# Performance work log

Measured on AMD Instinct MI355X. Metric: run time of the kernel, lower is better.

The kernel has to match this reference:

```python
import jax, jax.numpy as jnp
import numpy as np

B = 8
INPUT_DIM = 6670   # upper-triangle of 116x116 FC matrix (AAL atlas)
N = 116
FD = 16
HEADS = (8, 4, 1)
DIMS = (128, 256, 512)
NC = 2
THR = 0.5
EPS = 1e-5


def _glorot(key, shape):
    s = (2.0 / (shape[0] + shape[-1])) ** 0.5
    return jax.random.normal(key, shape, dtype=jnp.float32) * s


def setup_inputs() -> dict:
    key = jax.random.key(0)
    ks = iter(jax.random.split(key, 64))
    inp = {}
    inp['x'] = jax.random.normal(next(ks), (B, INPUT_DIM), dtype=jnp.float32)
    # DynamicGraphBuilder params
    inp['W_gb'] = _glorot(next(ks), (INPUT_DIM, N * N))
    inp['b_gb'] = jnp.zeros((N * N,), jnp.float32)
    inp['fe_W1'] = _glorot(next(ks), (2, 8)); inp['fe_b1'] = jnp.zeros((8,), jnp.float32)
    inp['fe_W2'] = _glorot(next(ks), (8, FD)); inp['fe_b2'] = jnp.zeros((FD,), jnp.float32)
    inp['ln_g'] = jnp.ones((FD,), jnp.float32); inp['ln_b'] = jnp.zeros((FD,), jnp.float32)
    # GATv2 layers
    prev = FD
    for l, (d, h) in enumerate(zip(DIMS, HEADS)):
        inp['Wl%d' % l] = _glorot(next(ks), (prev, h * d))
        inp['bl%d' % l] = jnp.zeros((h * d,), jnp.float32)
        inp['Wr%d' % l] = _glorot(next(ks), (prev, h * d))
        inp['br%d' % l] = jnp.zeros((h * d,), jnp.float32)
        inp['att%d' % l] = _glorot(next(ks), (h, d))
        inp['bias%d' % l] = jnp.zeros((h * d,), jnp.float32)
        prev = h * d
    # classifier
    inp['Wc1'] = _glorot(next(ks), (prev, 256)); inp['bc1'] = jnp.zeros((256,), jnp.float32)
    inp['bn_g'] = jnp.ones((256,), jnp.float32); inp['bn_b'] = jnp.zeros((256,), jnp.float32)
    inp['Wc2'] = _glorot(next(ks), (256, NC)); inp['bc2'] = jnp.zeros((NC,), jnp.float32)
    return inp


def _gatv2(hx, mask_st, Wl, bl, Wr, br, att, bias, heads, out_dim, self_loops):
    # mask_st[b, src, tgt] True if edge src->tgt exists (PyG flow source_to_target)
    Bn, Nn, _ = hx.shape
    if self_loops:  # PyG remove_self_loops + add_self_loops => diag forced present
        mask_st = mask_st | jnp.eye(Nn, dtype=bool)
    xl = (hx @ Wl + bl).reshape(Bn, Nn, heads, out_dim)  # source transform
    xr = (hx @ Wr + br).reshape(Bn, Nn, heads, out_dim)  # target transform
    # pairwise: axis1 = target i, axis2 = source j  -> [B, i, j, h, o]
    z = jax.nn.leaky_relu(xr[:, :, None] + xl[:, None, :], 0.2)
    e = jnp.einsum('bijho,ho->bhij', z, att)  # [B, h, tgt, src]
    m = jnp.swapaxes(mask_st, 1, 2)[:, None]  # [B, 1, tgt, src]
    em = jnp.where(m, e, -1e30)
    emax = jnp.max(em, axis=-1, keepdims=True)
    p = jnp.exp(em - emax) * m  # zero for masked / empty rows
    alpha = p / jnp.maximum(p.sum(-1, keepdims=True), 1e-16)
    out = jnp.einsum('bhij,bjho->biho', alpha, xl).reshape(Bn, Nn, heads * out_dim)
    return out + bias


def _forward(x, W_gb, b_gb, fe_W1, fe_b1, fe_W2, fe_b2, ln_g, ln_b,
             Wl0, bl0, Wr0, br0, att0, bias0,
             Wl1, bl1, Wr1, br1, att1, bias1,
             Wl2, bl2, Wr2, br2, att2, bias2,
             Wc1, bc1, bn_g, bn_b, Wc2, bc2):
    Bn = x.shape[0]
    adj = jax.nn.sigmoid(x @ W_gb + b_gb).reshape(Bn, N, N)
    mask = adj > THR                      # edge (row -> col) exists
    adj_t = jnp.where(mask, adj, 0.0)     # thresholded adjacency
    mu = adj_t.mean(-1)                   # torch mean(dim=1) on [N,N]
    std = jnp.sqrt(jnp.sum((adj_t - mu[..., None]) ** 2, -1) / (N - 1))  # unbiased
    stats = jnp.stack([mu, std], -1)      # [B, N, 2]
    hfe = jax.nn.gelu(stats @ fe_W1 + fe_b1, approximate=False) @ fe_W2 + fe_b2
    lm = hfe.mean(-1, keepdims=True)
    lv = jnp.mean((hfe - lm) ** 2, -1, keepdims=True)
    h = (hfe - lm) / jnp.sqrt(lv + EPS) * ln_g + ln_b  # [B, N, FD]
    convs = [
        (Wl0, bl0, Wr0, br0, att0, bias0, HEADS[0], DIMS[0], False),
        (Wl1, bl1, Wr1, br1, att1, bias1, HEADS[1], DIMS[1], True),
        (Wl2, bl2, Wr2, br2, att2, bias2, HEADS[2], DIMS[2], True),
    ]
    for (Wl, bl, Wr, br, att, bias, hh, dd, sl) in convs:
        h = jax.nn.gelu(_gatv2(h, mask, Wl, bl, Wr, br, att, bias, hh, dd, sl), approximate=False)
    pooled = h.mean(1)                    # global_mean_pool per graph
    c = pooled @ Wc1 + bc1
    c = c / jnp.sqrt(1.0 + EPS) * bn_g + bn_b  # BatchNorm1d eval (running mean 0, var 1)
    c = jax.nn.gelu(c, approximate=False)
    return c @ Wc2 + bc2


def reference(x, W_gb, b_gb, fe_W1, fe_b1, fe_W2, fe_b2, ln_g, ln_b,
              Wl0, bl0, Wr0, br0, att0, bias0,
              Wl1, bl1, Wr1, br1, att1, bias1,
              Wl2, bl2, Wr2, br2, att2, bias2,
              Wc1, bc1, bn_g, bn_b, Wc2, bc2):
    return _forward(x, W_gb, b_gb, fe_W1, fe_b1, fe_W2, fe_b2, ln_g, ln_b,
                    Wl0, bl0, Wr0, br0, att0, bias0,
                    Wl1, bl1, Wr1, br1, att1, bias1,
                    Wl2, bl2, Wr2, br2, att2, bias2,
                    Wc1, bc1, bn_g, bn_b, Wc2, bc2)
```

## Files before the change

kernel.cpp:

```cpp
#include <hip/hip_runtime.h>
#include <math.h>


#define NB 8
#define NN 116
#define NN2 (NN*NN)
#define KIN 6670
#define FD 16
#define KCHUNK 64
#define KSTEP 105

__device__ __forceinline__ float gelu_f(float x) {
  return 0.5f * x * (1.0f + erff(x * 0.70710678118654752f));
}
__device__ __forceinline__ float lrelu(float x) {
  return fmaxf(x, 0.2f * x);
}

__global__ __launch_bounds__(256) void k_gemm_big(
    const float* __restrict__ x, const float* __restrict__ Wg,
    float* __restrict__ partial) {
  int c0 = (blockIdx.x * 256 + threadIdx.x) * 4;
  if (c0 >= NN2) return;
  int chunk = blockIdx.y;
  int k0 = chunk * KSTEP;
  int k1 = min(k0 + KSTEP, KIN);
  float acc[NB][4];
#pragma unroll
  for (int b = 0; b < NB; b++)
#pragma unroll
    for (int c = 0; c < 4; c++) acc[b][c] = 0.f;
#pragma unroll 8
  for (int k = k0; k < k1; ++k) {
    float4 wv = *(const float4*)(Wg + (size_t)k * NN2 + c0);
    float w[4] = {wv.x, wv.y, wv.z, wv.w};
    float xs[NB];
#pragma unroll
    for (int b = 0; b < NB; b++) xs[b] = x[b * KIN + k];
#pragma unroll
    for (int b = 0; b < NB; b++)
#pragma unroll
      for (int c = 0; c < 4; c++)
        acc[b][c] = fmaf(xs[b], w[c], acc[b][c]);
  }
#pragma unroll
  for (int b = 0; b < NB; b++)
#pragma unroll
    for (int c = 0; c < 4; c++)
      partial[((size_t)chunk * NB + b) * NN2 + c0 + c] = acc[b][c];
}

__global__ void k_reduce_sigmoid(const float* __restrict__ partial,
                                 const float* __restrict__ bgb,
                                 float* __restrict__ adj) {
  int t = blockIdx.x * 256 + threadIdx.x;
  if (t >= NB * NN2) return;
  int b = t / NN2, rc = t % NN2;
  float s = bgb[rc];
#pragma unroll 8
  for (int ch = 0; ch < KCHUNK; ch++)
    s += partial[((size_t)ch * NB + b) * NN2 + rc];
  adj[t] = 1.0f / (1.0f + expf(-s));
}

__global__ void k_stats(const float* __restrict__ adj,
                        const float* __restrict__ feW1, const float* __restrict__ feb1,
                        const float* __restrict__ feW2, const float* __restrict__ feb2,
                        const float* __restrict__ lng, const float* __restrict__ lnb,
                        float* __restrict__ h0) {
  int b = blockIdx.x;
  int r = threadIdx.x;
  if (r >= NN) return;
  const float* row = adj + (size_t)(b * NN + r) * NN;
  float sum = 0.f;
  for (int c = 0; c < NN; c++) { float a = row[c]; sum += (a > 0.5f) ? a : 0.f; }
  float mu = sum / (float)NN;
  float ss = 0.f;
  for (int c = 0; c < NN; c++) {
    float a = row[c]; float m = (a > 0.5f) ? a : 0.f;
    float d = m - mu; ss += d * d;
  }
  float sd = sqrtf(ss / (float)(NN - 1));
  float hid[8];
#pragma unroll
  for (int a = 0; a < 8; a++) {
    float z = mu * feW1[a] + sd * feW1[8 + a] + feb1[a];
    hid[a] = gelu_f(z);
  }
  float hf[FD];
  float lm = 0.f;
#pragma unroll
  for (int o = 0; o < FD; o++) {
    float z = feb2[o];
#pragma unroll
    for (int a = 0; a < 8; a++) z += hid[a] * feW2[a * FD + o];
    hf[o] = z; lm += z;
  }
  lm /= (float)FD;
  float lv = 0.f;
#pragma unroll
  for (int o = 0; o < FD; o++) { float d = hf[o] - lm; lv += d * d; }
  lv /= (float)FD;
  float inv = 1.0f / sqrtf(lv + 1e-5f);
#pragma unroll
  for (int o = 0; o < FD; o++)
    h0[(size_t)(b * NN + r) * FD + o] = (hf[o] - lm) * inv * lng[o] + lnb[o];
}

#define GN 64
#define GK 32
template<int GM_, int TM_>
__global__ __launch_bounds__(256) void k_gemm_dual(
    const float* __restrict__ A,
    const float* __restrict__ W0, const float* __restrict__ b0,
    const float* __restrict__ W1, const float* __restrict__ b1,
    float* __restrict__ C0, float* __restrict__ C1,
    int M, int K, int N) {
  int nc = blockIdx.x * GN;
  const float* W    = (nc < N) ? W0 : W1;
  const float* bias = (nc < N) ? b0 : b1;
  float*       C    = (nc < N) ? C0 : C1;
  int n0 = (nc < N) ? nc : nc - N;
  int m0 = blockIdx.y * GM_;

  __shared__ float a_s[GK][GM_];
  __shared__ float b_s[GK][GN + 4];
  int t = threadIdx.x;
  int tx = t & 15, ty = t >> 4;
  float acc[TM_][4];
#pragma unroll
  for (int i = 0; i < TM_; i++)
#pragma unroll
    for (int j = 0; j < 4; j++) acc[i][j] = 0.f;

  constexpr int EPT = GM_ * GK / 256;

  for (int kt = 0; kt < K; kt += GK) {
    {
      int m = t & (GM_ - 1), kq = (t / GM_) * EPT;
      int gm = m0 + m;
      if (gm < M && (kt + kq + EPT) <= K) {
#pragma unroll
        for (int e = 0; e < EPT; e += 4) {
          float4 v = *(const float4*)(A + (size_t)gm * K + kt + kq + e);
          a_s[kq + e + 0][m] = v.x; a_s[kq + e + 1][m] = v.y;
          a_s[kq + e + 2][m] = v.z; a_s[kq + e + 3][m] = v.w;
        }
      } else {
#pragma unroll
        for (int e = 0; e < EPT; e++) {
          int gk = kt + kq + e;
          a_s[kq + e][m] = (gm < M && gk < K) ? A[(size_t)gm * K + gk] : 0.f;
        }
      }
    }
    {
      int k = t >> 3, n8 = (t & 7) * 8;
      int gk = kt + k;
      float4 w0 = make_float4(0.f,0.f,0.f,0.f), w1 = w0;
      if (gk < K) {
        const float* wp = W + (size_t)gk * N + n0 + n8;
        w0 = *(const float4*)(wp);
        w1 = *(const float4*)(wp + 4);
      }
      b_s[k][n8 + 0] = w0.x; b_s[k][n8 + 1] = w0.y;
      b_s[k][n8 + 2] = w0.z; b_s[k][n8 + 3] = w0.w;
      b_s[k][n8 + 4] = w1.x; b_s[k][n8 + 5] = w1.y;
      b_s[k][n8 + 6] = w1.z; b_s[k][n8 + 7] = w1.w;
    }
    __syncthreads();
#pragma unroll
    for (int kk = 0; kk < GK; kk++) {
      float4 bv = *(const float4*)(&b_s[kk][tx << 2]);
      float bn_[4] = {bv.x, bv.y, bv.z, bv.w};
#pragma unroll
      for (int r = 0; r < TM_ / 4; r++) {
        float4 av = *(const float4*)(&a_s[kk][ty * TM_ + r * 4]);
        float am[4] = {av.x, av.y, av.z, av.w};
#pragma unroll
        for (int i = 0; i < 4; i++)
#pragma unroll
          for (int j = 0; j < 4; j++)
            acc[r * 4 + i][j] = fmaf(am[i], bn_[j], acc[r * 4 + i][j]);
      }
    }
    __syncthreads();
  }
#pragma unroll
  for (int i = 0; i < TM_; i++) {
    int m = m0 + ty * TM_ + i;
    if (m >= M) break;
#pragma unroll
    for (int j = 0; j < 4; j++) {
      int n = n0 + (tx << 2) + j;
      C[(size_t)m * N + n] = acc[i][j] + bias[n];
    }
  }
}

template<int HH_, int DD_>
__global__ __launch_bounds__(512) void k_attn_aggr(
    const float* __restrict__ xl, const float* __restrict__ xr,
    const float* __restrict__ adj, const float* __restrict__ att,
    const float* __restrict__ bias, float* __restrict__ hout, int selfloop) {
  constexpr int HD = HH_ * DD_;
  __shared__ float xr_lds[4][HD];
  __shared__ float att_lds[HD];
  __shared__ __align__(16) float e_lds[HH_][128][4];
  __shared__ float maskf[4][128];
  int i0 = blockIdx.x * 4, b = blockIdx.y;
  int t = threadIdx.x;

  for (int idx = t; idx < HD; idx += 512) {
    att_lds[idx] = att[idx];
#pragma unroll
    for (int ti = 0; ti < 4; ti++)
      xr_lds[ti][idx] = xr[(size_t)(b * NN + i0 + ti) * HD + idx];
  }
  if (t < 128) {
#pragma unroll
    for (int ti = 0; ti < 4; ti++) {
      int i = i0 + ti;
      bool mj = (t < NN) && ((adj[(size_t)(b * NN + t) * NN + i] > 0.5f) ||
                             (selfloop && (t == i)));
      maskf[ti][t] = mj ? 1.f : 0.f;
    }
  }
  __syncthreads();

  int slice = t >> 7;
  int j = t & 127;
  bool valid = (j < NN);
  const float* xlj = xl + (size_t)(b * NN + (valid ? j : 0)) * HD;
  if constexpr (HH_ >= 4) {
    constexpr int HQ = HH_ / 4;
#pragma unroll
    for (int hh = 0; hh < HQ; hh++) {
      int h = slice * HQ + hh;
      int base = h * DD_;
      float acc[4] = {0.f, 0.f, 0.f, 0.f};
      for (int o = 0; o < DD_; o += 4) {
        float4 v  = *(const float4*)(xlj + base + o);
        float4 af = *(const float4*)(att_lds + base + o);
#pragma unroll
        for (int ti = 0; ti < 4; ti++) {
          float4 r = *(const float4*)(&xr_lds[ti][base + o]);
          float a = acc[ti];
          a = fmaf(af.x, lrelu(r.x + v.x), a);
          a = fmaf(af.y, lrelu(r.y + v.y), a);
          a = fmaf(af.z, lrelu(r.z + v.z), a);
          a = fmaf(af.w, lrelu(r.w + v.w), a);
          acc[ti] = a;
        }
      }
      if (valid)
        *(float4*)(&e_lds[h][j][0]) = make_float4(acc[0], acc[1], acc[2], acc[3]);
    }
    __syncthreads();
  } else {
    constexpr int DH = DD_ / 2;
    float acc[4] = {0.f, 0.f, 0.f, 0.f};
    if (slice < 2) {
      int base = slice * DH;
      for (int o = 0; o < DH; o += 4) {
        float4 v  = *(const float4*)(xlj + base + o);
        float4 af = *(const float4*)(att_lds + base + o);
#pragma unroll
        for (int ti = 0; ti < 4; ti++) {
          float4 r = *(const float4*)(&xr_lds[ti][base + o]);
          float a = acc[ti];
          a = fmaf(af.x, lrelu(r.x + v.x), a);
          a = fmaf(af.y, lrelu(r.y + v.y), a);
          a = fmaf(af.z, lrelu(r.z + v.z), a);
          a = fmaf(af.w, lrelu(r.w + v.w), a);
          acc[ti] = a;
        }
      }
    }
    if (slice == 0 && valid)
      *(float4*)(&e_lds[0][j][0]) = make_float4(acc[0], acc[1], acc[2], acc[3]);
    __syncthreads();
    if (slice == 1 && valid) {
      float4 p = *(const float4*)(&e_lds[0][j][0]);
      p.x += acc[0]; p.y += acc[1]; p.z += acc[2]; p.w += acc[3];
      *(float4*)(&e_lds[0][j][0]) = p;
    }
    __syncthreads();
  }

  {
    int w = t >> 6, lane = t & 63;
    for (int fh = w; fh < 4 * HH_; fh += 8) {
      int ti = fh / HH_, h = fh - ti * HH_;
      float mk0 = maskf[ti][lane], mk1 = maskf[ti][lane + 64];
      float e0 = e_lds[h][lane][ti], e1 = e_lds[h][lane + 64][ti];
      float v = fmaxf(mk0 != 0.f ? e0 : -3.0e38f,
                      mk1 != 0.f ? e1 : -3.0e38f);
#pragma unroll
      for (int o = 32; o; o >>= 1) v = fmaxf(v, __shfl_xor(v, o, 64));
      float p0 = (mk0 != 0.f) ? expf(e0 - v) : 0.f;
      float p1 = (mk1 != 0.f) ? expf(e1 - v) : 0.f;
      float s = p0 + p1;
#pragma unroll
      for (int o = 32; o; o >>= 1) s += __shfl_xor(s, o, 64);
      float inv = 1.0f / fmaxf(s, 1e-16f);
      e_lds[h][lane][ti]      = p0 * inv;
      e_lds[h][lane + 64][ti] = p1 * inv;
    }
  }
  __syncthreads();

  constexpr int CITER = HD / 512;
  const float* xb = xl + (size_t)b * NN * HD;
  float* hb = hout + (size_t)(b * NN + i0) * HD;
#pragma unroll
  for (int it = 0; it < CITER; it++) {
    int c = t + (it << 9);
    int h = c / DD_;
    const float* xp = xb + c;
    float a0 = 0.f, a1 = 0.f, a2 = 0.f, a3 = 0.f;
#pragma unroll 4
    for (int jj = 0; jj < NN; jj++) {
      float xv = xp[(size_t)jj * HD];
      float4 al = *(const float4*)(&e_lds[h][jj][0]);
      a0 = fmaf(al.x, xv, a0);
      a1 = fmaf(al.y, xv, a1);
      a2 = fmaf(al.z, xv, a2);
      a3 = fmaf(al.w, xv, a3);
    }
    float bv = bias[c];
    hb[c]          = gelu_f(a0 + bv);
    hb[HD + c]     = gelu_f(a1 + bv);
    hb[2 * HD + c] = gelu_f(a2 + bv);
    hb[3 * HD + c] = gelu_f(a3 + bv);
  }
}

__global__ __launch_bounds__(256) void k_classifier(
    const float* __restrict__ hfin,
    const float* __restrict__ Wc1, const float* __restrict__ bc1,
    const float* __restrict__ bng, const float* __restrict__ bnb,
    const float* __restrict__ Wc2, const float* __restrict__ bc2,
    float* __restrict__ out) {
  __shared__ float pooled[512];
  __shared__ float cls[256];
  int b = blockIdx.x;
  int t = threadIdx.x;
#pragma unroll
  for (int r = 0; r < 2; r++) {
    int c = t + (r << 8);
    float s = 0.f;
    for (int i = 0; i < NN; i++) s += hfin[(size_t)(b * NN + i) * 512 + c];
    pooled[c] = s / (float)NN;
  }
  __syncthreads();
  {
    int n = t;
    float acc = bc1[n];
    for (int k = 0; k < 512; k++)
      acc = fmaf(pooled[k], Wc1[k * 256 + n], acc);
    float c = acc * (1.0f / sqrtf(1.0f + 1e-5f)) * bng[n] + bnb[n];
    cls[n] = gelu_f(c);
  }
  __syncthreads();
  if (t < 128) {
    int jj = t >> 6, lane = t & 63;
    float s = 0.f;
#pragma unroll
    for (int w = 0; w < 4; w++) {
      int k = lane + (w << 6);
      s += cls[k] * Wc2[k * 2 + jj];
    }
#pragma unroll
    for (int o = 32; o; o >>= 1) s += __shfl_xor(s, o, 64);
    if (lane == 0) out[b * 2 + jj] = s + bc2[jj];
  }
}

extern "C" void kernel_launch(void* const* d_in, const int* in_sizes, int n_in,
                              void* d_out, int out_size, void* d_ws, size_t ws_size,
                              hipStream_t stream) {
  const float* x    = (const float*)d_in[0];
  const float* Wgb  = (const float*)d_in[1];
  const float* bgb  = (const float*)d_in[2];
  const float* feW1 = (const float*)d_in[3];
  const float* feb1 = (const float*)d_in[4];
  const float* feW2 = (const float*)d_in[5];
  const float* feb2 = (const float*)d_in[6];
  const float* lng  = (const float*)d_in[7];
  const float* lnb  = (const float*)d_in[8];
  const float* Wl[3]   = {(const float*)d_in[9],  (const float*)d_in[15], (const float*)d_in[21]};
  const float* bl[3]   = {(const float*)d_in[10], (const float*)d_in[16], (const float*)d_in[22]};
  const float* Wr[3]   = {(const float*)d_in[11], (const float*)d_in[17], (const float*)d_in[23]};
  const float* br[3]   = {(const float*)d_in[12], (const float*)d_in[18], (const float*)d_in[24]};
  const float* att[3]  = {(const float*)d_in[13], (const float*)d_in[19], (const float*)d_in[25]};
  const float* bias[3] = {(const float*)d_in[14], (const float*)d_in[20], (const float*)d_in[26]};
  const float* Wc1 = (const float*)d_in[27];
  const float* bc1 = (const float*)d_in[28];
  const float* bng = (const float*)d_in[29];
  const float* bnb = (const float*)d_in[30];
  const float* Wc2 = (const float*)d_in[31];
  const float* bc2 = (const float*)d_in[32];

  float* ws = (float*)d_ws;
  float* adj = ws + 53376;
  float* scratch = ws + 161024;
  float* partial = scratch;
  float* hA      = scratch;
  float* hB      = hA + 950272;
  float* xlbuf   = hB + 950272;
  float* xrbuf   = xlbuf + 950272;

  k_gemm_big<<<dim3(14, KCHUNK), 256, 0, stream>>>(x, Wgb, partial);
  k_reduce_sigmoid<<<dim3((NB * NN2 + 255) / 256), 256, 0, stream>>>(partial, bgb, adj);
  k_stats<<<dim3(NB), 128, 0, stream>>>(adj, feW1, feb1, feW2, feb2, lng, lnb, hA);

  dim3 ab(NN / 4, NB);
  k_gemm_dual<64, 4><<<dim3(2 * 1024 / GN, 15), 256, 0, stream>>>(
      hA, Wl[0], bl[0], Wr[0], br[0], xlbuf, xrbuf, 928, 16, 1024);
  k_attn_aggr<8, 128><<<ab, 512, 0, stream>>>(xlbuf, xrbuf, adj, att[0], bias[0], hB, 0);
  k_gemm_dual<128, 8><<<dim3(2 * 1024 / GN, 8), 256, 0, stream>>>(
      hB, Wl[1], bl[1], Wr[1], br[1], xlbuf, xrbuf, 928, 1024, 1024);
  k_attn_aggr<4, 256><<<ab, 512, 0, stream>>>(xlbuf, xrbuf, adj, att[1], bias[1], hA, 1);
  k_gemm_dual<64, 4><<<dim3(2 * 512 / GN, 15), 256, 0, stream>>>(
      hA, Wl[2], bl[2], Wr[2], br[2], xlbuf, xrbuf, 928, 1024, 512);
  k_attn_aggr<1, 512><<<ab, 512, 0, stream>>>(xlbuf, xrbuf, adj, att[2], bias[2], hB, 1);

  k_classifier<<<dim3(NB), 256, 0, stream>>>(hB, Wc1, bc1, bng, bnb, Wc2, bc2,
                                             (float*)d_out);
}
```

Baseline: 895.4 us.

## Double-buffer dual GEMM, stage x in LDS, halve attention target tile

Adds a register-prefetch double-buffered dual GEMM for layers 1 and 2, switching layer 1 from 128-row to 64-row tiles. The big graph-builder GEMM now stages its x slice in shared memory once per block instead of every thread loading it from global memory. The attention kernel now handles 2 targets per block instead of 4, doubling grid size but re-reading xl twice as often. It also simplifies the layer-0 A loader to scalar loads and unrolls the classifier loop. The double-buffered kernel assumes 928 rows fit its tiles and that K is a multiple of 32.

```diff
diff --git a/kernel.cpp b/kernel.cpp
--- a/kernel.cpp
+++ b/kernel.cpp
@@ -20,10 +20,18 @@
 __global__ __launch_bounds__(256) void k_gemm_big(
     const float* __restrict__ x, const float* __restrict__ Wg,
     float* __restrict__ partial) {
-  int c0 = (blockIdx.x * 256 + threadIdx.x) * 4;
-  if (c0 >= NN2) return;
+  __shared__ float xs_lds[KSTEP][8];
+  int t = threadIdx.x;
   int chunk = blockIdx.y;
   int k0 = chunk * KSTEP;
+  for (int e = t; e < KSTEP * 8; e += 256) {
+    int kk = e >> 3, bb = e & 7;
+    int gk = k0 + kk;
+    xs_lds[kk][bb] = (gk < KIN) ? x[bb * KIN + gk] : 0.f;
+  }
+  __syncthreads();
+  int c0 = (blockIdx.x * 256 + t) * 4;
+  if (c0 >= NN2) return;
   int k1 = min(k0 + KSTEP, KIN);
   float acc[NB][4];
 #pragma unroll
@@ -33,10 +41,10 @@
 #pragma unroll 8
   for (int k = k0; k < k1; ++k) {
     float4 wv = *(const float4*)(Wg + (size_t)k * NN2 + c0);
+    float4 xa = *(const float4*)(&xs_lds[k - k0][0]);
+    float4 xb = *(const float4*)(&xs_lds[k - k0][4]);
     float w[4] = {wv.x, wv.y, wv.z, wv.w};
-    float xs[NB];
-#pragma unroll
-    for (int b = 0; b < NB; b++) xs[b] = x[b * KIN + k];
+    float xs[NB] = {xa.x, xa.y, xa.z, xa.w, xb.x, xb.y, xb.z, xb.w};
 #pragma unroll
     for (int b = 0; b < NB; b++)
 #pragma unroll
@@ -110,7 +118,7 @@
 #define GN 64
 #define GK 32
 template<int GM_, int TM_>
-__global__ __launch_bounds__(256) void k_gemm_dual(
+__global__ __launch_bounds__(256) void k_gemm_dual_s(
     const float* __restrict__ A,
     const float* __restrict__ W0, const float* __restrict__ b0,
     const float* __restrict__ W1, const float* __restrict__ b1,
@@ -139,19 +147,10 @@
     {
       int m = t & (GM_ - 1), kq = (t / GM_) * EPT;
       int gm = m0 + m;
-      if (gm < M && (kt + kq + EPT) <= K) {
-#pragma unroll
-        for (int e = 0; e < EPT; e += 4) {
-          float4 v = *(const float4*)(A + (size_t)gm * K + kt + kq + e);
-          a_s[kq + e + 0][m] = v.x; a_s[kq + e + 1][m] = v.y;
-          a_s[kq + e + 2][m] = v.z; a_s[kq + e + 3][m] = v.w;
-        }
-      } else {
-#pragma unroll
-        for (int e = 0; e < EPT; e++) {
-          int gk = kt + kq + e;
-          a_s[kq + e][m] = (gm < M && gk < K) ? A[(size_t)gm * K + gk] : 0.f;
-        }
+#pragma unroll
+      for (int e = 0; e < EPT; e++) {
+        int gk = kt + kq + e;
+        a_s[kq + e][m] = (gm < M && gk < K) ? A[(size_t)gm * K + gk] : 0.f;
       }
     }
     {
@@ -198,28 +197,130 @@
   }
 }
 
+template<int GM_, int TM_>
+__global__ __launch_bounds__(256) void k_gemm_dual_db(
+    const float* __restrict__ A,
+    const float* __restrict__ W0, const float* __restrict__ b0,
+    const float* __restrict__ W1, const float* __restrict__ b1,
+    float* __restrict__ C0, float* __restrict__ C1,
+    int M, int K, int N) {
+  int nc = blockIdx.x * GN;
+  const float* W    = (nc < N) ? W0 : W1;
+  const float* bias = (nc < N) ? b0 : b1;
+  float*       C    = (nc < N) ? C0 : C1;
+  int n0 = (nc < N) ? nc : nc - N;
+  int m0 = blockIdx.y * GM_;
+
+  __shared__ float a_s[2][GK][GM_];
+  __shared__ float b_s[2][GK][GN + 4];
+  int t = threadIdx.x;
+  int tx = t & 15, ty = t >> 4;
+  constexpr int EPT = GM_ * GK / 256;
+  constexpr int NF4 = EPT / 4;
+  int ms = t & (GM_ - 1);
+  int kq = (t / GM_) * EPT;
+  int gm = m0 + ms;
+  int kb = t >> 3;
+  int n8 = (t & 7) * 8;
+  const float* arow = A + (size_t)gm * K;
+
+  float4 ra[NF4];
+  float4 rb0, rb1;
+
+  auto LOAD = [&](int kt) {
+#pragma unroll
+    for (int r = 0; r < NF4; r++)
+      ra[r] = (gm < M) ? *(const float4*)(arow + kt + kq + 4 * r)
+                       : make_float4(0.f, 0.f, 0.f, 0.f);
+    const float* wp = W + (size_t)(kt + kb) * N + n0 + n8;
+    rb0 = *(const float4*)(wp);
+    rb1 = *(const float4*)(wp + 4);
+  };
+  auto STORE = [&](int buf) {
+#pragma unroll
+    for (int r = 0; r < NF4; r++) {
+      a_s[buf][kq + 4 * r + 0][ms] = ra[r].x;
+      a_s[buf][kq + 4 * r + 1][ms] = ra[r].y;
+      a_s[buf][kq + 4 * r + 2][ms] = ra[r].z;
+      a_s[buf][kq + 4 * r + 3][ms] = ra[r].w;
+    }
+    b_s[buf][kb][n8 + 0] = rb0.x; b_s[buf][kb][n8 + 1] = rb0.y;
+    b_s[buf][kb][n8 + 2] = rb0.z; b_s[buf][kb][n8 + 3] = rb0.w;
+    b_s[buf][kb][n8 + 4] = rb1.x; b_s[buf][kb][n8 + 5] = rb1.y;
+    b_s[buf][kb][n8 + 6] = rb1.z; b_s[buf][kb][n8 + 7] = rb1.w;
+  };
+
+  float acc[TM_][4];
+#pragma unroll
+  for (int i = 0; i < TM_; i++)
+#pragma unroll
+    for (int j = 0; j < 4; j++) acc[i][j] = 0.f;
+
+  auto COMPUTE = [&](int buf) {
+#pragma unroll
+    for (int kk = 0; kk < GK; kk++) {
+      float4 bv = *(const float4*)(&b_s[buf][kk][tx << 2]);
+      float bn_[4] = {bv.x, bv.y, bv.z, bv.w};
+#pragma unroll
+      for (int r = 0; r < TM_ / 4; r++) {
+        float4 av = *(const float4*)(&a_s[buf][kk][ty * TM_ + 4 * r]);
+        float am[4] = {av.x, av.y, av.z, av.w};
+#pragma unroll
+        for (int i = 0; i < 4; i++)
+#pragma unroll
+          for (int j = 0; j < 4; j++)
+            acc[r * 4 + i][j] = fmaf(am[i], bn_[j], acc[r * 4 + i][j]);
+      }
+    }
+  };
+
+  int nt = K / GK;
+  LOAD(0); STORE(0);
+  __syncthreads();
+  int cur = 0;
+  for (int it = 1; it < nt; it++) {
+    LOAD(it * GK);
+    COMPUTE(cur);
+    __syncthreads();
+    STORE(cur ^ 1);
+    __syncthreads();
+    cur ^= 1;
+  }
+  COMPUTE(cur);
+
+#pragma unroll
+  for (int i = 0; i < TM_; i++) {
+    int m = m0 + ty * TM_ + i;
+    if (m >= M) break;
+#pragma unroll
+    for (int j = 0; j < 4; j++) {
+      int n = n0 + (tx << 2) + j;
+      C[(size_t)m * N + n] = acc[i][j] + bias[n];
+    }
+  }
+}
+
 template<int HH_, int DD_>
 __global__ __launch_bounds__(512) void k_attn_aggr(
     const float* __restrict__ xl, const float* __restrict__ xr,
     const float* __restrict__ adj, const float* __restrict__ att,
     const float* __restrict__ bias, float* __restrict__ hout, int selfloop) {
   constexpr int HD = HH_ * DD_;
-  __shared__ float xr_lds[4][HD];
+  __shared__ float xr_lds[2][HD];
   __shared__ float att_lds[HD];
-  __shared__ __align__(16) float e_lds[HH_][128][4];
-  __shared__ float maskf[4][128];
-  int i0 = blockIdx.x * 4, b = blockIdx.y;
+  __shared__ __align__(16) float e_lds[HH_][128][2];
+  __shared__ float maskf[2][128];
+  int i0 = blockIdx.x * 2, b = blockIdx.y;
   int t = threadIdx.x;
 
   for (int idx = t; idx < HD; idx += 512) {
     att_lds[idx] = att[idx];
-#pragma unroll
-    for (int ti = 0; ti < 4; ti++)
-      xr_lds[ti][idx] = xr[(size_t)(b * NN + i0 + ti) * HD + idx];
+    xr_lds[0][idx] = xr[(size_t)(b * NN + i0) * HD + idx];
+    xr_lds[1][idx] = xr[(size_t)(b * NN + i0 + 1) * HD + idx];
   }
   if (t < 128) {
 #pragma unroll
-    for (int ti = 0; ti < 4; ti++) {
+    for (int ti = 0; ti < 2; ti++) {
       int i = i0 + ti;
       bool mj = (t < NN) && ((adj[(size_t)(b * NN + t) * NN + i] > 0.5f) ||
                              (selfloop && (t == i)));
@@ -238,59 +339,53 @@
     for (int hh = 0; hh < HQ; hh++) {
       int h = slice * HQ + hh;
       int base = h * DD_;
-      float acc[4] = {0.f, 0.f, 0.f, 0.f};
+      float a0 = 0.f, a1 = 0.f;
       for (int o = 0; o < DD_; o += 4) {
         float4 v  = *(const float4*)(xlj + base + o);
         float4 af = *(const float4*)(att_lds + base + o);
-#pragma unroll
-        for (int ti = 0; ti < 4; ti++) {
-          float4 r = *(const float4*)(&xr_lds[ti][base + o]);
-          float a = acc[ti];
-          a = fmaf(af.x, lrelu(r.x + v.x), a);
-          a = fmaf(af.y, lrelu(r.y + v.y), a);
-          a = fmaf(af.z, lrelu(r.z + v.z), a);
-          a = fmaf(af.w, lrelu(r.w + v.w), a);
-          acc[ti] = a;
-        }
+        float4 r0 = *(const float4*)(&xr_lds[0][base + o]);
+        float4 r1 = *(const float4*)(&xr_lds[1][base + o]);
+        a0 = fmaf(af.x, lrelu(r0.x + v.x), a0);
+        a0 = fmaf(af.y, lrelu(r0.y + v.y), a0);
+        a0 = fmaf(af.z, lrelu(r0.z + v.z), a0);
+        a0 = fmaf(af.w, lrelu(r0.w + v.w), a0);
+        a1 = fmaf(af.x, lrelu(r1.x + v.x), a1);
+        a1 = fmaf(af.y, lrelu(r1.y + v.y), a1);
+        a1 = fmaf(af.z, lrelu(r1.z + v.z), a1);
+        a1 = fmaf(af.w, lrelu(r1.w + v.w), a1);
       }
-      if (valid)
-        *(float4*)(&e_lds[h][j][0]) = make_float4(acc[0], acc[1], acc[2], acc[3]);
+      if (valid) { e_lds[h][j][0] = a0; e_lds[h][j][1] = a1; }
     }
     __syncthreads();
   } else {
     constexpr int DH = DD_ / 2;
-    float acc[4] = {0.f, 0.f, 0.f, 0.f};
+    float a0 = 0.f, a1 = 0.f;
     if (slice < 2) {
       int base = slice * DH;
       for (int o = 0; o < DH; o += 4) {
         float4 v  = *(const float4*)(xlj + base + o);
         float4 af = *(const float4*)(att_lds + base + o);
-#pragma unroll
-        for (int ti = 0; ti < 4; ti++) {
-          float4 r = *(const float4*)(&xr_lds[ti][base + o]);
-          float a = acc[ti];
-          a = fmaf(af.x, lrelu(r.x + v.x), a);
-          a = fmaf(af.y, lrelu(r.y + v.y), a);
-          a = fmaf(af.z, lrelu(r.z + v.z), a);
-          a = fmaf(af.w, lrelu(r.w + v.w), a);
-          acc[ti] = a;
-        }
+        float4 r0 = *(const float4*)(&xr_lds[0][base + o]);
+        float4 r1 = *(const float4*)(&xr_lds[1][base + o]);
+        a0 = fmaf(af.x, lrelu(r0.x + v.x), a0);
+        a0 = fmaf(af.y, lrelu(r0.y + v.y), a0);
+        a0 = fmaf(af.z, lrelu(r0.z + v.z), a0);
+        a0 = fmaf(af.w, lrelu(r0.w + v.w), a0);
+        a1 = fmaf(af.x, lrelu(r1.x + v.x), a1);
+        a1 = fmaf(af.y, lrelu(r1.y + v.y), a1);
+        a1 = fmaf(af.z, lrelu(r1.z + v.z), a1);
+        a1 = fmaf(af.w, lrelu(r1.w + v.w), a1);
       }
     }
-    if (slice == 0 && valid)
-      *(float4*)(&e_lds[0][j][0]) = make_float4(acc[0], acc[1], acc[2], acc[3]);
-    __syncthreads();
-    if (slice == 1 && valid) {
-      float4 p = *(const float4*)(&e_lds[0][j][0]);
-      p.x += acc[0]; p.y += acc[1]; p.z += acc[2]; p.w += acc[3];
-      *(float4*)(&e_lds[0][j][0]) = p;
-    }
+    if (slice == 0 && valid) { e_lds[0][j][0] = a0; e_lds[0][j][1] = a1; }
+    __syncthreads();
+    if (slice == 1 && valid) { e_lds[0][j][0] += a0; e_lds[0][j][1] += a1; }
     __syncthreads();
   }
 
   {
     int w = t >> 6, lane = t & 63;
-    for (int fh = w; fh < 4 * HH_; fh += 8) {
+    for (int fh = w; fh < 2 * HH_; fh += 8) {
       int ti = fh / HH_, h = fh - ti * HH_;
       float mk0 = maskf[ti][lane], mk1 = maskf[ti][lane + 64];
       float e0 = e_lds[h][lane][ti], e1 = e_lds[h][lane + 64][ti];
@@ -318,21 +413,17 @@
     int c = t + (it << 9);
     int h = c / DD_;
     const float* xp = xb + c;
-    float a0 = 0.f, a1 = 0.f, a2 = 0.f, a3 = 0.f;
+    float a0 = 0.f, a1 = 0.f;
 #pragma unroll 4
     for (int jj = 0; jj < NN; jj++) {
       float xv = xp[(size_t)jj * HD];
-      float4 al = *(const float4*)(&e_lds[h][jj][0]);
+      float2 al = *(const float2*)(&e_lds[h][jj][0]);
       a0 = fmaf(al.x, xv, a0);
       a1 = fmaf(al.y, xv, a1);
-      a2 = fmaf(al.z, xv, a2);
-      a3 = fmaf(al.w, xv, a3);
     }
     float bv = bias[c];
-    hb[c]          = gelu_f(a0 + bv);
-    hb[HD + c]     = gelu_f(a1 + bv);
-    hb[2 * HD + c] = gelu_f(a2 + bv);
-    hb[3 * HD + c] = gelu_f(a3 + bv);
+    hb[c]      = gelu_f(a0 + bv);
+    hb[HD + c] = gelu_f(a1 + bv);
   }
 }
 
@@ -357,6 +448,7 @@
   {
     int n = t;
     float acc = bc1[n];
+#pragma unroll 8
     for (int k = 0; k < 512; k++)
       acc = fmaf(pooled[k], Wc1[k * 256 + n], acc);
     float c = acc * (1.0f / sqrtf(1.0f + 1e-5f)) * bng[n] + bnb[n];
@@ -415,14 +507,14 @@
   k_reduce_sigmoid<<<dim3((NB * NN2 + 255) / 256), 256, 0, stream>>>(partial, bgb, adj);
   k_stats<<<dim3(NB), 128, 0, stream>>>(adj, feW1, feb1, feW2, feb2, lng, lnb, hA);
 
-  dim3 ab(NN / 4, NB);
-  k_gemm_dual<64, 4><<<dim3(2 * 1024 / GN, 15), 256, 0, stream>>>(
+  dim3 ab(NN / 2, NB);
+  k_gemm_dual_s<64, 4><<<dim3(2 * 1024 / GN, 15), 256, 0, stream>>>(
       hA, Wl[0], bl[0], Wr[0], br[0], xlbuf, xrbuf, 928, 16, 1024);
   k_attn_aggr<8, 128><<<ab, 512, 0, stream>>>(xlbuf, xrbuf, adj, att[0], bias[0], hB, 0);
-  k_gemm_dual<128, 8><<<dim3(2 * 1024 / GN, 8), 256, 0, stream>>>(
+  k_gemm_dual_db<64, 4><<<dim3(2 * 1024 / GN, 15), 256, 0, stream>>>(
       hB, Wl[1], bl[1], Wr[1], br[1], xlbuf, xrbuf, 928, 1024, 1024);
   k_attn_aggr<4, 256><<<ab, 512, 0, stream>>>(xlbuf, xrbuf, adj, att[1], bias[1], hA, 1);
-  k_gemm_dual<64, 4><<<dim3(2 * 512 / GN, 15), 256, 0, stream>>>(
+  k_gemm_dual_db<64, 4><<<dim3(2 * 512 / GN, 15), 256, 0, stream>>>(
       hA, Wl[2], bl[2], Wr[2], br[2], xlbuf, xrbuf, 928, 1024, 512);
   k_attn_aggr<1, 512><<<ab, 512, 0, stream>>>(xlbuf, xrbuf, adj, att[2], bias[2], hB, 1);
 
```

Measured after the change: 858.3 us. 1.04x faster.
